# Kernel optimization log

Hardware: AMD Instinct MI355X
Metric: run time of the kernel (lower is better)

The kernel has to match this reference:

```python
import jax, jax.numpy as jnp
import numpy as np

FRACTION = 0.33  # from attn_type='query_selector_0.33'


def setup_inputs() -> dict:
    key = jax.random.key(0)
    k1, k2, k3, k4 = jax.random.split(key, 4)
    B, L, DIM_VAL, DIM_ATTN = 8, 4096, 64, 64
    scale = 1.0 / np.sqrt(DIM_VAL).astype(np.float32)
    x = jax.random.normal(k1, (B, L, DIM_VAL), dtype=jnp.float32)
    Wq = jax.random.normal(k2, (DIM_VAL, DIM_ATTN), dtype=jnp.float32) * scale
    Wk = jax.random.normal(k3, (DIM_VAL, DIM_ATTN), dtype=jnp.float32) * scale
    Wv = jax.random.normal(k4, (DIM_VAL, DIM_VAL), dtype=jnp.float32) * scale
    return {"x": x, "Wq": Wq, "Wk": Wk, "Wv": Wv}


def reference(x, Wq, Wk, Wv):
    # Projections (bias-free Linears)
    Q = jnp.einsum('bld,de->ble', x, Wq)  # [B, L, Da]
    K = jnp.einsum('bld,de->ble', x, Wk)  # [B, L, Da]
    V = jnp.einsum('bld,de->ble', x, Wv)  # [B, L, Dv]

    B, L_Q, Da = Q.shape
    l_Q = int((1.0 - FRACTION) * L_Q)  # static: shapes known at trace time

    # keys.topk(l_Q, dim=1).values -> per-channel top-l_Q along seq; mean over them
    K_top = jax.lax.top_k(jnp.swapaxes(K, 1, 2), l_Q)[0]  # [B, Da, l_Q]
    K_reduce = K_top.mean(axis=-1)                         # [B, Da]

    # score each query against the reduced key; pick top-l_Q queries
    sqk = jnp.einsum('bd,bld->bl', K_reduce, Q)            # [B, L_Q]
    indices = jax.lax.top_k(sqk, l_Q)[1]                   # [B, l_Q] int32

    # gather sampled queries
    Q_sample = jnp.take_along_axis(Q, indices[:, :, None], axis=1)  # [B, l_Q, Da]

    # dense attention for the sampled queries only
    scores = jnp.einsum('bqd,bkd->bqk', Q_sample, K) / jnp.sqrt(jnp.asarray(Da, Q.dtype))
    attn = jax.nn.softmax(scores, axis=-1)                 # [B, l_Q, L]
    out_sel = jnp.einsum('bqk,bkv->bqv', attn, V)          # [B, l_Q, Dv]

    # mean-filled result, scatter attention outputs to selected rows
    mean_values = V.mean(axis=-2)                          # [B, Dv]
    result = jnp.broadcast_to(mean_values[:, None, :], (B, L_Q, V.shape[-1]))
    result = result.at[jnp.arange(B)[:, None], indices].set(out_sel)
    return result
```

## Files before the change

### kernel.cpp

```cpp
#include <hip/hip_runtime.h>
#include <hip/hip_bf16.h>
#include <math.h>

#define BATCH 8
#define SEQ   4096
#define DIM   64
#define LQ    2744
#define QPB   128
#define NQB   22
#define QPAD  2816
#define KS    4
#define QSC   0.1803368801111204f

typedef _Float16 half8 __attribute__((ext_vector_type(8)));
typedef short    bs8   __attribute__((ext_vector_type(8)));
typedef float    fx16  __attribute__((ext_vector_type(16)));
typedef unsigned short ushort_t;

union UH { uint4 u4; half8 h; };
union UB { unsigned u[4]; uint4 u4; bs8 s; };

__device__ __forceinline__ unsigned pack_bf16(float a, float b) {
    __hip_bfloat162 h = __float22bfloat162_rn(make_float2(a, b));
    union { __hip_bfloat162 h; unsigned u; } cv; cv.h = h; return cv.u;
}

__device__ __forceinline__ unsigned f2sort(float f) {
    unsigned u = __float_as_uint(f);
    return (u & 0x80000000u) ? ~u : (u | 0x80000000u);
}
__device__ __forceinline__ float sort2f(unsigned u) {
    return __uint_as_float((u & 0x80000000u) ? (u & 0x7FFFFFFFu) : ~u);
}

struct RadSh {
    unsigned u[4096];
    unsigned hist[256];
    unsigned wsum[4];
    unsigned res[2];
    float    rsum[4];
    int      eq[256];
    int      cnts[2];
};

__device__ void radix_select_4096(const unsigned* u, int k, unsigned* hist,
                                  unsigned* wsum, unsigned* res, int pass_lo) {
    const int t = threadIdx.x;
    const int lane = t & 63, wv = t >> 6;
    if (t == 0) { res[0] = 0u; res[1] = (unsigned)k; }
    for (int pass = 3; pass >= pass_lo; --pass) {
        const int shift = pass * 8;
        hist[t] = 0u;
        __syncthreads();
        const unsigned pref  = res[0];
        const unsigned kk    = res[1];
        const unsigned hmask = (pass == 3) ? 0u : (0xFFFFFFFFu << (shift + 8));
        for (int i = t; i < 4096; i += 256) {
            unsigned ui = u[i];
            if ((ui & hmask) == pref) atomicAdd(&hist[(ui >> shift) & 255u], 1u);
        }
        __syncthreads();
        const unsigned h = hist[t];
        unsigned s = h;
#pragma unroll
        for (int ofs = 1; ofs < 64; ofs <<= 1) {
            unsigned a = __shfl_down(s, ofs, 64);
            s += (lane + ofs < 64) ? a : 0u;
        }
        if (lane == 0) wsum[wv] = s;
        __syncthreads();
#pragma unroll
        for (int w2 = 0; w2 < 4; ++w2)
            if (w2 > wv) s += wsum[w2];
        if (s >= kk && (s - h) < kk) {
            res[0] = pref | ((unsigned)t << shift);
            res[1] = kk - (s - h);
        }
        __syncthreads();
    }
}

__global__ __launch_bounds__(256) void proj_kernel(
    const float* __restrict__ x,  const float* __restrict__ Wq,
    const float* __restrict__ Wk, const float* __restrict__ Wv,
    float* __restrict__ Q, float* __restrict__ Kt,
    _Float16* __restrict__ Qh, _Float16* __restrict__ Kh,
    ushort_t* __restrict__ Vt, float* __restrict__ pmean) {
    const int rt = blockIdx.x, b = blockIdx.y, t = threadIdx.x;
    __shared__ float  red[4][64];
    const int ch = t & 63, rg = t >> 6;
    const float* xb = x + (size_t)b * SEQ * DIM;
    float accq[16], acck[16], accv[16];
#pragma unroll
    for (int i = 0; i < 16; ++i) { accq[i] = 0.f; acck[i] = 0.f; accv[i] = 0.f; }
    for (int dc = 0; dc < 4; ++dc) {
        float wq[16], wk[16], wv[16];
#pragma unroll
        for (int dd = 0; dd < 16; ++dd) {
            int d = dc * 16 + dd;
            wq[dd] = Wq[d * 64 + ch]; wk[dd] = Wk[d * 64 + ch]; wv[dd] = Wv[d * 64 + ch];
        }
        for (int r = 0; r < 16; ++r) {
            const int off = (rt * 64 + rg * 16 + r) * DIM + dc * 16;
            const float* xrow =
                xb + (unsigned)__builtin_amdgcn_readfirstlane(off);
            float xv[16];
#pragma unroll
            for (int dd = 0; dd < 16; ++dd) xv[dd] = xrow[dd];
#pragma unroll
            for (int dd = 0; dd < 16; ++dd) {
                accq[r] = fmaf(xv[dd], wq[dd], accq[r]);
                acck[r] = fmaf(xv[dd], wk[dd], acck[r]);
                accv[r] = fmaf(xv[dd], wv[dd], accv[r]);
            }
        }
    }
    const int rowbase = rt * 64 + rg * 16;
    float sv = 0.f;
#pragma unroll
    for (int r = 0; r < 16; ++r) {
        size_t o = ((size_t)b * SEQ + rowbase + r) * DIM + ch;
        Q[o]  = accq[r];
        Qh[o] = (_Float16)(accq[r] * QSC);
        Kh[o] = (_Float16)acck[r];
        sv += accv[r];
    }
    float4* ktp = (float4*)(Kt + ((size_t)b * 64 + ch) * SEQ + rowbase);
    ktp[0] = make_float4(acck[0], acck[1], acck[2], acck[3]);
    ktp[1] = make_float4(acck[4], acck[5], acck[6], acck[7]);
    ktp[2] = make_float4(acck[8], acck[9], acck[10], acck[11]);
    ktp[3] = make_float4(acck[12], acck[13], acck[14], acck[15]);
    {
        unsigned pk[8];
#pragma unroll
        for (int i = 0; i < 8; ++i) pk[i] = pack_bf16(accv[2*i], accv[2*i+1]);
        uint4* vp = (uint4*)(Vt + ((size_t)(b * 64 + ch)) * SEQ + rowbase);
        vp[0] = make_uint4(pk[0], pk[1], pk[4], pk[5]);
        vp[1] = make_uint4(pk[2], pk[3], pk[6], pk[7]);
    }
    red[rg][ch] = sv;
    __syncthreads();
    if (rg == 0)
        pmean[((size_t)b * 64 + ch) * 64 + rt] =
            red[0][ch] + red[1][ch] + red[2][ch] + red[3][ch];
}

__global__ __launch_bounds__(256) void kmean_kernel(const float* __restrict__ Kt,
                                                    const float* __restrict__ pmean,
                                                    float* __restrict__ Kred,
                                                    float* __restrict__ meanfin) {
    __shared__ RadSh sh;
    const int bc = blockIdx.x, t = threadIdx.x;
    if (t < 64) {
        float v = pmean[(size_t)bc * 64 + t];
        for (int m = 1; m < 64; m <<= 1) v += __shfl_xor(v, m, 64);
        if (t == 0) meanfin[bc] = v * (1.0f / (float)SEQ);
    }
    const float4* c4 = (const float4*)(Kt + (size_t)bc * SEQ);
    for (int i = t; i < 1024; i += 256) {
        float4 v = c4[i];
        sh.u[i*4+0] = f2sort(v.x); sh.u[i*4+1] = f2sort(v.y);
        sh.u[i*4+2] = f2sort(v.z); sh.u[i*4+3] = f2sort(v.w);
    }
    __syncthreads();
    radix_select_4096(sh.u, LQ, sh.hist, sh.wsum, sh.res, 2);
    const unsigned Tu = sh.res[0];
    const int krem = (int)sh.res[1];
    float loc = 0.f;
    for (int i = t; i < 4096; i += 256)
        if ((sh.u[i] & 0xFFFF0000u) > Tu) loc += sort2f(sh.u[i]);
    for (int msk = 1; msk < 64; msk <<= 1) loc += __shfl_xor(loc, msk, 64);
    if ((t & 63) == 0) sh.rsum[t >> 6] = loc;
    __syncthreads();
    if (t == 0) {
        float s = sh.rsum[0] + sh.rsum[1] + sh.rsum[2] + sh.rsum[3]
                + (float)krem * sort2f(Tu | 0x8000u);
        Kred[bc] = s / (float)LQ;
    }
}

__global__ __launch_bounds__(256) void sqk_kernel(const float* __restrict__ Q,
                                                  const float* __restrict__ Kred,
                                                  float* __restrict__ sqk,
                                                  float4* __restrict__ pz) {
    const int b = blockIdx.y, l = blockIdx.x * 256 + threadIdx.x;
    __shared__ float kr[64];
    if (threadIdx.x < 64) kr[threadIdx.x] = Kred[b * 64 + threadIdx.x];
    {
        const int tid = (blockIdx.y * 16 + blockIdx.x) * 256 + threadIdx.x;
        const float4 z = make_float4(0.f, 0.f, 0.f, 0.f);
        for (int i = tid; i < 366080; i += 32768) pz[i] = z;
    }
    __syncthreads();
    const float4* q = (const float4*)(Q + ((size_t)b * SEQ + l) * DIM);
    float s = 0.f;
#pragma unroll
    for (int i = 0; i < 16; ++i) {
        float4 v = q[i];
        s = fmaf(v.x, kr[i*4+0], s); s = fmaf(v.y, kr[i*4+1], s);
        s = fmaf(v.z, kr[i*4+2], s); s = fmaf(v.w, kr[i*4+3], s);
    }
    sqk[b * SEQ + l] = s;
}

__global__ __launch_bounds__(256) void select_kernel(const float* __restrict__ sqk,
                                                     int* __restrict__ sel,
                                                     int* __restrict__ inv) {
    __shared__ RadSh r;
    const int b = blockIdx.x, t = threadIdx.x;
    const float* col = sqk + (size_t)b * SEQ;
    int* invb = inv + (size_t)b * SEQ;
    for (int i = t; i < 4096; i += 256) {
        r.u[i] = f2sort(col[i]);
        invb[i] = -1;
    }
    if (t < 2) r.cnts[t] = 0;
    __syncthreads();
    radix_select_4096(r.u, LQ, r.hist, r.wsum, r.res, 0);
    const unsigned Tu = r.res[0];
    const int krem = (int)r.res[1];
    int* selb = sel + b * QPAD;
    for (int i = t; i < 4096; i += 256) {
        unsigned ui = r.u[i];
        if (ui > Tu) {
            int p = atomicAdd(&r.cnts[0], 1);
            selb[p] = i;
            invb[i] = p;
        } else if (ui == Tu) {
            int p = atomicAdd(&r.cnts[1], 1);
            if (p < 256) r.eq[p] = i;
        }
    }
    __syncthreads();
    if (t == 0) {
        int ng = r.cnts[0];
        int ne = r.cnts[1] < 256 ? r.cnts[1] : 256;
        for (int i = 1; i < ne; ++i) {
            int v = r.eq[i], j = i - 1;
            while (j >= 0 && r.eq[j] > v) { r.eq[j+1] = r.eq[j]; --j; }
            r.eq[j+1] = v;
        }
        for (int j = 0; j < krem; ++j) {
            selb[ng + j] = r.eq[j];
            invb[r.eq[j]] = ng + j;
        }
    }
    __syncthreads();
    if (t < QPAD - LQ) selb[LQ + t] = selb[LQ - 1];
}

__global__ __launch_bounds__(256, 3) void attn_kernel(
    const ushort_t* __restrict__ Qh, const ushort_t* __restrict__ Kh,
    const ushort_t* __restrict__ Vt, const int* __restrict__ sel,
    float* __restrict__ pl, float* __restrict__ pout) {
    const int qt = blockIdx.x, ks = blockIdx.y, b = blockIdx.z;
    const int t = threadIdx.x, w = t >> 6, lane = t & 63;
    const int col = lane & 31, h = lane >> 5;

    __shared__ ushort_t Ktile[2][32 * 64];
    __shared__ ushort_t Vtile[2][32 * 64];

    half8 qf[4];
    {
        const int q = qt * QPB + w * 32 + col;
        const int row = sel[b * QPAD + q];
        const uint4* qg = (const uint4*)(Qh + ((size_t)b * SEQ + row) * DIM);
#pragma unroll
        for (int m = 0; m < 4; ++m) { UH u; u.u4 = qg[2 * m + h]; qf[m] = u.h; }
    }

    int koff[4], voff[4];
#pragma unroll
    for (int m = 0; m < 4; ++m)
        koff[m] = col * 64 + 8 * ((2 * m + h) ^ (col & 7));
#pragma unroll
    for (int i = 0; i < 4; ++i)
        voff[i] = col * 64 + 8 * ((i * 2 + h) ^ (col & 7));

    fx16 O0, O1;
#pragma unroll
    for (int r = 0; r < 16; ++r) { O0[r] = 0.f; O1[r] = 0.f; }
    float l = 0.f;

    const int srow = t >> 3, sgr = t & 7;
    const int lg = sgr ^ (srow & 7);
    const int vD = lg >> 2, vc = (lg >> 1) & 1, vh = lg & 1;
    const size_t kgbase = ((size_t)b * SEQ + ks * 1024 + srow) * DIM + 8 * lg;
    const size_t vgbase = ((size_t)(b * DIM + srow + 32 * vD)) * SEQ
                          + ks * 1024 + vc * 16 + vh * 8;

    const int sw = srow * 64 + sgr * 8;

    auto step = [&](int buf) {
        fx16 S;
#pragma unroll
        for (int r = 0; r < 16; ++r) S[r] = 0.f;
#pragma unroll
        for (int m = 0; m < 4; ++m) {
            UH kf;
            kf.u4 = *(const uint4*)&Ktile[buf][koff[m]];
            S = __builtin_amdgcn_mfma_f32_32x32x16_f16(kf.h, qf[m], S, 0, 0, 0);
        }
        float p[16];
#pragma unroll
        for (int r = 0; r < 16; ++r) p[r] = exp2f(S[r]);
#pragma unroll
        for (int r = 0; r < 16; ++r) l += p[r];
        UB A0, A1;
#pragma unroll
        for (int v = 0; v < 4; ++v) {
            A0.u[v] = pack_bf16(p[2 * v],     p[2 * v + 1]);
            A1.u[v] = pack_bf16(p[8 + 2 * v], p[8 + 2 * v + 1]);
        }
#pragma unroll
        for (int D = 0; D < 2; ++D) {
            fx16& O = D ? O1 : O0;
#pragma unroll
            for (int c = 0; c < 2; ++c) {
                UB vf;
                vf.u4 = *(const uint4*)&Vtile[buf][voff[D * 2 + c]];
                O = __builtin_amdgcn_mfma_f32_32x32x16_bf16(c ? A1.s : A0.s, vf.s,
                                                            O, 0, 0, 0);
            }
        }
    };

    uint4 kA = *(const uint4*)(Kh + kgbase);
    uint4 vA = *(const uint4*)(Vt + vgbase);
    uint4 kB = *(const uint4*)(Kh + kgbase + 32 * DIM);
    uint4 vB = *(const uint4*)(Vt + vgbase + 32);

    for (int tile = 0; tile < 32; tile += 2) {
        *(uint4*)&Ktile[0][sw] = kA;
        *(uint4*)&Vtile[0][sw] = vA;
        __syncthreads();
        if (tile + 2 < 32) {
            kA = *(const uint4*)(Kh + kgbase + (size_t)(tile + 2) * 32 * DIM);
            vA = *(const uint4*)(Vt + vgbase + (size_t)(tile + 2) * 32);
        }
        step(0);
        *(uint4*)&Ktile[1][sw] = kB;
        *(uint4*)&Vtile[1][sw] = vB;
        __syncthreads();
        if (tile + 3 < 32) {
            kB = *(const uint4*)(Kh + kgbase + (size_t)(tile + 3) * 32 * DIM);
            vB = *(const uint4*)(Vt + vgbase + (size_t)(tile + 3) * 32);
        }
        step(1);
    }

    l += __shfl_xor(l, 32);

    const int qg0 = qt * QPB + w * 32;
    const size_t base = (size_t)b * QPAD + qg0;
#pragma unroll
    for (int D = 0; D < 2; ++D) {
        const fx16& O = D ? O1 : O0;
#pragma unroll
        for (int r = 0; r < 16; ++r) {
            const int q = (r & 3) + 8 * (r >> 2) + 4 * h;
            atomicAdd(&pout[(base + q) * DIM + D * 32 + col], O[r]);
        }
    }
    if (h == 0) atomicAdd(&pl[base + col], l);
}

__global__ __launch_bounds__(256) void comb_kernel(
    const float* __restrict__ pl, const float* __restrict__ pout,
    const int* __restrict__ inv, const float* __restrict__ meanfin,
    float* __restrict__ out) {
    const int idx = blockIdx.x * 256 + threadIdx.x;
    const int b = idx >> 16;
    const int rc = idx & 65535;
    const int row = rc >> 4, c = rc & 15;
    const int p = inv[b * SEQ + row];
    float4 o;
    if (p >= 0) {
        const size_t s0 = (size_t)b * QPAD + p;
        const float invl = 1.0f / pl[s0];
        float4 a = ((const float4*)(pout + s0 * DIM))[c];
        o = make_float4(a.x * invl, a.y * invl, a.z * invl, a.w * invl);
    } else {
        o = make_float4(meanfin[b * 64 + c * 4 + 0], meanfin[b * 64 + c * 4 + 1],
                        meanfin[b * 64 + c * 4 + 2], meanfin[b * 64 + c * 4 + 3]);
    }
    ((float4*)out)[idx] = o;
}

extern "C" void kernel_launch(void* const* d_in, const int* in_sizes, int n_in,
                              void* d_out, int out_size, void* d_ws, size_t ws_size,
                              hipStream_t stream) {
    const float* x  = (const float*)d_in[0];
    const float* Wq = (const float*)d_in[1];
    const float* Wk = (const float*)d_in[2];
    const float* Wv = (const float*)d_in[3];
    float* out = (float*)d_out;
    char* wsb  = (char*)d_ws;

    float*    Q       = (float*)(wsb);
    _Float16* Qh      = (_Float16*)(wsb + 8388608);
    _Float16* Kh      = (_Float16*)(wsb + 12582912);
    ushort_t* Vt      = (ushort_t*)(wsb + 16777216);
    float*    pmean   = (float*)(wsb + 20971520);
    float*    meanfin = (float*)(wsb + 21102592);
    float*    Kred    = (float*)(wsb + 21104640);
    float*    sqk     = (float*)(wsb + 21106688);
    int*      sel     = (int*)(wsb + 21237760);
    int*      inv     = (int*)(wsb + 21327872);
    float*    Kt      = (float*)(wsb + 21458944);
    float*    pout    = (float*)(wsb + 21458944);
    float*    pl      = (float*)(wsb + 21458944 + 5767168);

    proj_kernel  <<<dim3(64, 8),          256, 0, stream>>>(x, Wq, Wk, Wv, Q, Kt,
                                                            Qh, Kh, Vt, pmean);
    kmean_kernel <<<512,                  256, 0, stream>>>(Kt, pmean, Kred, meanfin);
    sqk_kernel   <<<dim3(16, 8),          256, 0, stream>>>(Q, Kred, sqk,
                                                            (float4*)pout);
    select_kernel<<<8,                    256, 0, stream>>>(sqk, sel, inv);
    attn_kernel  <<<dim3(NQB, KS, BATCH), 256, 0, stream>>>((const ushort_t*)Qh,
                                                            (const ushort_t*)Kh,
                                                            Vt, sel, pl, pout);
    comb_kernel  <<<2048,                 256, 0, stream>>>(pl, pout, inv, meanfin, out);
}
```

Baseline: 183.3 us.

## Fuse query scoring into selection kernel and move zero-fill into kmean

The separate sqk and select kernels become one 1024-thread-per-batch kernel. It computes the query scores directly into shared memory and runs the radix select there, so the global sqk buffer and one launch go away. The radix select now takes a configurable thread count. Zeroing of the partial-output buffer moves into kmean_kernel: each block clears the Kt slice it has already copied to shared memory, which aliases pout. The attention step also starts its first MFMA from a zero register instead of a cleared accumulator and sums the row probabilities as a tree. The cost is that the score computation now runs on only 8 blocks, which may limit the memory bandwidth available for reading Q.

```diff
diff --git a/kernel.cpp b/kernel.cpp
--- a/kernel.cpp
+++ b/kernel.cpp
@@ -44,37 +44,43 @@
 };
 
 __device__ void radix_select_4096(const unsigned* u, int k, unsigned* hist,
-                                  unsigned* wsum, unsigned* res, int pass_lo) {
+                                  unsigned* wsum, unsigned* res, int pass_lo,
+                                  int NT) {
     const int t = threadIdx.x;
     const int lane = t & 63, wv = t >> 6;
     if (t == 0) { res[0] = 0u; res[1] = (unsigned)k; }
     for (int pass = 3; pass >= pass_lo; --pass) {
         const int shift = pass * 8;
-        hist[t] = 0u;
+        if (t < 256) hist[t] = 0u;
         __syncthreads();
         const unsigned pref  = res[0];
         const unsigned kk    = res[1];
         const unsigned hmask = (pass == 3) ? 0u : (0xFFFFFFFFu << (shift + 8));
-        for (int i = t; i < 4096; i += 256) {
+        for (int i = t; i < 4096; i += NT) {
             unsigned ui = u[i];
             if ((ui & hmask) == pref) atomicAdd(&hist[(ui >> shift) & 255u], 1u);
         }
         __syncthreads();
-        const unsigned h = hist[t];
-        unsigned s = h;
-#pragma unroll
-        for (int ofs = 1; ofs < 64; ofs <<= 1) {
-            unsigned a = __shfl_down(s, ofs, 64);
-            s += (lane + ofs < 64) ? a : 0u;
-        }
-        if (lane == 0) wsum[wv] = s;
-        __syncthreads();
-#pragma unroll
-        for (int w2 = 0; w2 < 4; ++w2)
-            if (w2 > wv) s += wsum[w2];
-        if (s >= kk && (s - h) < kk) {
-            res[0] = pref | ((unsigned)t << shift);
-            res[1] = kk - (s - h);
+        unsigned h = 0u, s = 0u;
+        if (t < 256) {
+            h = hist[t];
+            s = h;
+#pragma unroll
+            for (int ofs = 1; ofs < 64; ofs <<= 1) {
+                unsigned a = __shfl_down(s, ofs, 64);
+                s += (lane + ofs < 64) ? a : 0u;
+            }
+            if (lane == 0) wsum[wv] = s;
+        }
+        __syncthreads();
+        if (t < 256) {
+#pragma unroll
+            for (int w2 = 0; w2 < 4; ++w2)
+                if (w2 > wv) s += wsum[w2];
+            if (s >= kk && (s - h) < kk) {
+                res[0] = pref | ((unsigned)t << shift);
+                res[1] = kk - (s - h);
+            }
         }
         __syncthreads();
     }
@@ -145,7 +151,7 @@
             red[0][ch] + red[1][ch] + red[2][ch] + red[3][ch];
 }
 
-__global__ __launch_bounds__(256) void kmean_kernel(const float* __restrict__ Kt,
+__global__ __launch_bounds__(256) void kmean_kernel(float* __restrict__ Kt,
                                                     const float* __restrict__ pmean,
                                                     float* __restrict__ Kred,
                                                     float* __restrict__ meanfin) {
@@ -163,7 +169,12 @@
         sh.u[i*4+2] = f2sort(v.z); sh.u[i*4+3] = f2sort(v.w);
     }
     __syncthreads();
-    radix_select_4096(sh.u, LQ, sh.hist, sh.wsum, sh.res, 2);
+    {
+        float4* pz = (float4*)Kt + (size_t)bc * 1024;
+        const float4 z = make_float4(0.f, 0.f, 0.f, 0.f);
+        for (int i = t; i < 1024; i += 256) pz[i] = z;
+    }
+    radix_select_4096(sh.u, LQ, sh.hist, sh.wsum, sh.res, 2, 256);
     const unsigned Tu = sh.res[0];
     const int krem = (int)sh.res[1];
     float loc = 0.f;
@@ -179,48 +190,35 @@
     }
 }
 
-__global__ __launch_bounds__(256) void sqk_kernel(const float* __restrict__ Q,
-                                                  const float* __restrict__ Kred,
-                                                  float* __restrict__ sqk,
-                                                  float4* __restrict__ pz) {
-    const int b = blockIdx.y, l = blockIdx.x * 256 + threadIdx.x;
+__global__ __launch_bounds__(1024) void sqk_select_kernel(
+    const float* __restrict__ Q, const float* __restrict__ Kred,
+    int* __restrict__ sel, int* __restrict__ inv) {
+    __shared__ RadSh r;
     __shared__ float kr[64];
-    if (threadIdx.x < 64) kr[threadIdx.x] = Kred[b * 64 + threadIdx.x];
-    {
-        const int tid = (blockIdx.y * 16 + blockIdx.x) * 256 + threadIdx.x;
-        const float4 z = make_float4(0.f, 0.f, 0.f, 0.f);
-        for (int i = tid; i < 366080; i += 32768) pz[i] = z;
-    }
-    __syncthreads();
-    const float4* q = (const float4*)(Q + ((size_t)b * SEQ + l) * DIM);
-    float s = 0.f;
-#pragma unroll
-    for (int i = 0; i < 16; ++i) {
-        float4 v = q[i];
-        s = fmaf(v.x, kr[i*4+0], s); s = fmaf(v.y, kr[i*4+1], s);
-        s = fmaf(v.z, kr[i*4+2], s); s = fmaf(v.w, kr[i*4+3], s);
-    }
-    sqk[b * SEQ + l] = s;
-}
-
-__global__ __launch_bounds__(256) void select_kernel(const float* __restrict__ sqk,
-                                                     int* __restrict__ sel,
-                                                     int* __restrict__ inv) {
-    __shared__ RadSh r;
     const int b = blockIdx.x, t = threadIdx.x;
-    const float* col = sqk + (size_t)b * SEQ;
+    if (t < 64) kr[t] = Kred[b * 64 + t];
     int* invb = inv + (size_t)b * SEQ;
-    for (int i = t; i < 4096; i += 256) {
-        r.u[i] = f2sort(col[i]);
-        invb[i] = -1;
+    __syncthreads();
+    for (int j = 0; j < 4; ++j) {
+        const int l = t + 1024 * j;
+        const float4* q = (const float4*)(Q + ((size_t)b * SEQ + l) * DIM);
+        float s = 0.f;
+#pragma unroll
+        for (int i = 0; i < 16; ++i) {
+            float4 v = q[i];
+            s = fmaf(v.x, kr[i*4+0], s); s = fmaf(v.y, kr[i*4+1], s);
+            s = fmaf(v.z, kr[i*4+2], s); s = fmaf(v.w, kr[i*4+3], s);
+        }
+        r.u[l] = f2sort(s);
+        invb[l] = -1;
     }
     if (t < 2) r.cnts[t] = 0;
     __syncthreads();
-    radix_select_4096(r.u, LQ, r.hist, r.wsum, r.res, 0);
+    radix_select_4096(r.u, LQ, r.hist, r.wsum, r.res, 0, 1024);
     const unsigned Tu = r.res[0];
     const int krem = (int)r.res[1];
     int* selb = sel + b * QPAD;
-    for (int i = t; i < 4096; i += 256) {
+    for (int i = t; i < 4096; i += 1024) {
         unsigned ui = r.u[i];
         if (ui > Tu) {
             int p = atomicAdd(&r.cnts[0], 1);
@@ -277,9 +275,9 @@
     for (int i = 0; i < 4; ++i)
         voff[i] = col * 64 + 8 * ((i * 2 + h) ^ (col & 7));
 
-    fx16 O0, O1;
-#pragma unroll
-    for (int r = 0; r < 16; ++r) { O0[r] = 0.f; O1[r] = 0.f; }
+    fx16 O0, O1, Zf;
+#pragma unroll
+    for (int r = 0; r < 16; ++r) { O0[r] = 0.f; O1[r] = 0.f; Zf[r] = 0.f; }
     float l = 0.f;
 
     const int srow = t >> 3, sgr = t & 7;
@@ -292,11 +290,10 @@
     const int sw = srow * 64 + sgr * 8;
 
     auto step = [&](int buf) {
-        fx16 S;
-#pragma unroll
-        for (int r = 0; r < 16; ++r) S[r] = 0.f;
-#pragma unroll
-        for (int m = 0; m < 4; ++m) {
+        UH kf0; kf0.u4 = *(const uint4*)&Ktile[buf][koff[0]];
+        fx16 S = __builtin_amdgcn_mfma_f32_32x32x16_f16(kf0.h, qf[0], Zf, 0, 0, 0);
+#pragma unroll
+        for (int m = 1; m < 4; ++m) {
             UH kf;
             kf.u4 = *(const uint4*)&Ktile[buf][koff[m]];
             S = __builtin_amdgcn_mfma_f32_32x32x16_f16(kf.h, qf[m], S, 0, 0, 0);
@@ -304,8 +301,13 @@
         float p[16];
 #pragma unroll
         for (int r = 0; r < 16; ++r) p[r] = exp2f(S[r]);
-#pragma unroll
-        for (int r = 0; r < 16; ++r) l += p[r];
+        {
+            float l01 = (p[0] + p[1]) + (p[2] + p[3]);
+            float l23 = (p[4] + p[5]) + (p[6] + p[7]);
+            float l45 = (p[8] + p[9]) + (p[10] + p[11]);
+            float l67 = (p[12] + p[13]) + (p[14] + p[15]);
+            l += (l01 + l23) + (l45 + l67);
+        }
         UB A0, A1;
 #pragma unroll
         for (int v = 0; v < 4; ++v) {
@@ -404,7 +406,6 @@
     float*    pmean   = (float*)(wsb + 20971520);
     float*    meanfin = (float*)(wsb + 21102592);
     float*    Kred    = (float*)(wsb + 21104640);
-    float*    sqk     = (float*)(wsb + 21106688);
     int*      sel     = (int*)(wsb + 21237760);
     int*      inv     = (int*)(wsb + 21327872);
     float*    Kt      = (float*)(wsb + 21458944);
@@ -414,9 +415,7 @@
     proj_kernel  <<<dim3(64, 8),          256, 0, stream>>>(x, Wq, Wk, Wv, Q, Kt,
                                                             Qh, Kh, Vt, pmean);
     kmean_kernel <<<512,                  256, 0, stream>>>(Kt, pmean, Kred, meanfin);
-    sqk_kernel   <<<dim3(16, 8),          256, 0, stream>>>(Q, Kred, sqk,
-                                                            (float4*)pout);
-    select_kernel<<<8,                    256, 0, stream>>>(sqk, sel, inv);
+    sqk_select_kernel<<<8,               1024, 0, stream>>>(Q, Kred, sel, inv);
     attn_kernel  <<<dim3(NQB, KS, BATCH), 256, 0, stream>>>((const ushort_t*)Qh,
                                                             (const ushort_t*)Kh,
                                                             Vt, sel, pl, pout);
```

Measured after the change: 215.0 us. 17.3% more time.

## Fuse combine step into attention via last-block scatter and mean prefill

Applied to the files above, without the earlier changes.

Removes the separate combine kernel and the inverse-index array. The sqk kernel now prefills the output with per-batch column means. The last attention block to finish each query tile, tracked by an atomic counter stored in the reused sqk buffer, normalizes the tile and scatters it into the selected rows. Zeroing of the partial-sum buffers moves from sqk_kernel into kmean_kernel, which overwrites its own Kt column after loading it. Minor tweaks add a tree-shaped row-sum and seed the first MFMA with a zero accumulator. In exchange the attention tail gains a threadfence, an extra barrier and a serialized epilogue.

```diff
diff --git a/kernel.cpp b/kernel.cpp
--- a/kernel.cpp
+++ b/kernel.cpp
@@ -145,7 +145,7 @@
             red[0][ch] + red[1][ch] + red[2][ch] + red[3][ch];
 }
 
-__global__ __launch_bounds__(256) void kmean_kernel(const float* __restrict__ Kt,
+__global__ __launch_bounds__(256) void kmean_kernel(float* __restrict__ Kt,
                                                     const float* __restrict__ pmean,
                                                     float* __restrict__ Kred,
                                                     float* __restrict__ meanfin) {
@@ -163,6 +163,11 @@
         sh.u[i*4+2] = f2sort(v.z); sh.u[i*4+3] = f2sort(v.w);
     }
     __syncthreads();
+    {
+        float4* pz = (float4*)Kt + (size_t)bc * 1024;
+        const float4 z = make_float4(0.f, 0.f, 0.f, 0.f);
+        for (int i = t; i < 1024; i += 256) pz[i] = z;
+    }
     radix_select_4096(sh.u, LQ, sh.hist, sh.wsum, sh.res, 2);
     const unsigned Tu = sh.res[0];
     const int krem = (int)sh.res[1];
@@ -182,15 +187,14 @@
 __global__ __launch_bounds__(256) void sqk_kernel(const float* __restrict__ Q,
                                                   const float* __restrict__ Kred,
                                                   float* __restrict__ sqk,
-                                                  float4* __restrict__ pz) {
+                                                  const float* __restrict__ meanf,
+                                                  float* __restrict__ out) {
     const int b = blockIdx.y, l = blockIdx.x * 256 + threadIdx.x;
     __shared__ float kr[64];
+    __shared__ float4 mf4[16];
     if (threadIdx.x < 64) kr[threadIdx.x] = Kred[b * 64 + threadIdx.x];
-    {
-        const int tid = (blockIdx.y * 16 + blockIdx.x) * 256 + threadIdx.x;
-        const float4 z = make_float4(0.f, 0.f, 0.f, 0.f);
-        for (int i = tid; i < 366080; i += 32768) pz[i] = z;
-    }
+    if (threadIdx.x < 16)
+        mf4[threadIdx.x] = ((const float4*)(meanf + b * 64))[threadIdx.x];
     __syncthreads();
     const float4* q = (const float4*)(Q + ((size_t)b * SEQ + l) * DIM);
     float s = 0.f;
@@ -201,21 +205,20 @@
         s = fmaf(v.z, kr[i*4+2], s); s = fmaf(v.w, kr[i*4+3], s);
     }
     sqk[b * SEQ + l] = s;
-}
-
-__global__ __launch_bounds__(256) void select_kernel(const float* __restrict__ sqk,
-                                                     int* __restrict__ sel,
-                                                     int* __restrict__ inv) {
+    float4* orow = (float4*)(out + ((size_t)b * SEQ + l) * DIM);
+#pragma unroll
+    for (int c = 0; c < 16; ++c) orow[c] = mf4[c];
+}
+
+__global__ __launch_bounds__(256) void select_kernel(float* __restrict__ sqk,
+                                                     int* __restrict__ sel) {
     __shared__ RadSh r;
     const int b = blockIdx.x, t = threadIdx.x;
     const float* col = sqk + (size_t)b * SEQ;
-    int* invb = inv + (size_t)b * SEQ;
-    for (int i = t; i < 4096; i += 256) {
-        r.u[i] = f2sort(col[i]);
-        invb[i] = -1;
-    }
+    for (int i = t; i < 4096; i += 256) r.u[i] = f2sort(col[i]);
     if (t < 2) r.cnts[t] = 0;
     __syncthreads();
+    if (t < NQB) ((int*)(sqk + (size_t)b * SEQ))[t] = 0;
     radix_select_4096(r.u, LQ, r.hist, r.wsum, r.res, 0);
     const unsigned Tu = r.res[0];
     const int krem = (int)r.res[1];
@@ -225,7 +228,6 @@
         if (ui > Tu) {
             int p = atomicAdd(&r.cnts[0], 1);
             selb[p] = i;
-            invb[i] = p;
         } else if (ui == Tu) {
             int p = atomicAdd(&r.cnts[1], 1);
             if (p < 256) r.eq[p] = i;
@@ -240,10 +242,7 @@
             while (j >= 0 && r.eq[j] > v) { r.eq[j+1] = r.eq[j]; --j; }
             r.eq[j+1] = v;
         }
-        for (int j = 0; j < krem; ++j) {
-            selb[ng + j] = r.eq[j];
-            invb[r.eq[j]] = ng + j;
-        }
+        for (int j = 0; j < krem; ++j) selb[ng + j] = r.eq[j];
     }
     __syncthreads();
     if (t < QPAD - LQ) selb[LQ + t] = selb[LQ - 1];
@@ -252,13 +251,15 @@
 __global__ __launch_bounds__(256, 3) void attn_kernel(
     const ushort_t* __restrict__ Qh, const ushort_t* __restrict__ Kh,
     const ushort_t* __restrict__ Vt, const int* __restrict__ sel,
-    float* __restrict__ pl, float* __restrict__ pout) {
+    float* __restrict__ pl, float* __restrict__ pout,
+    int* __restrict__ cnt, float* __restrict__ out) {
     const int qt = blockIdx.x, ks = blockIdx.y, b = blockIdx.z;
     const int t = threadIdx.x, w = t >> 6, lane = t & 63;
     const int col = lane & 31, h = lane >> 5;
 
     __shared__ ushort_t Ktile[2][32 * 64];
     __shared__ ushort_t Vtile[2][32 * 64];
+    __shared__ int amlast;
 
     half8 qf[4];
     {
@@ -277,9 +278,9 @@
     for (int i = 0; i < 4; ++i)
         voff[i] = col * 64 + 8 * ((i * 2 + h) ^ (col & 7));
 
-    fx16 O0, O1;
-#pragma unroll
-    for (int r = 0; r < 16; ++r) { O0[r] = 0.f; O1[r] = 0.f; }
+    fx16 O0, O1, Zf;
+#pragma unroll
+    for (int r = 0; r < 16; ++r) { O0[r] = 0.f; O1[r] = 0.f; Zf[r] = 0.f; }
     float l = 0.f;
 
     const int srow = t >> 3, sgr = t & 7;
@@ -292,11 +293,10 @@
     const int sw = srow * 64 + sgr * 8;
 
     auto step = [&](int buf) {
-        fx16 S;
-#pragma unroll
-        for (int r = 0; r < 16; ++r) S[r] = 0.f;
-#pragma unroll
-        for (int m = 0; m < 4; ++m) {
+        UH kf0; kf0.u4 = *(const uint4*)&Ktile[buf][koff[0]];
+        fx16 S = __builtin_amdgcn_mfma_f32_32x32x16_f16(kf0.h, qf[0], Zf, 0, 0, 0);
+#pragma unroll
+        for (int m = 1; m < 4; ++m) {
             UH kf;
             kf.u4 = *(const uint4*)&Ktile[buf][koff[m]];
             S = __builtin_amdgcn_mfma_f32_32x32x16_f16(kf.h, qf[m], S, 0, 0, 0);
@@ -304,8 +304,13 @@
         float p[16];
 #pragma unroll
         for (int r = 0; r < 16; ++r) p[r] = exp2f(S[r]);
-#pragma unroll
-        for (int r = 0; r < 16; ++r) l += p[r];
+        {
+            float l01 = (p[0] + p[1]) + (p[2] + p[3]);
+            float l23 = (p[4] + p[5]) + (p[6] + p[7]);
+            float l45 = (p[8] + p[9]) + (p[10] + p[11]);
+            float l67 = (p[12] + p[13]) + (p[14] + p[15]);
+            l += (l01 + l23) + (l45 + l67);
+        }
         UB A0, A1;
 #pragma unroll
         for (int v = 0; v < 4; ++v) {
@@ -363,28 +368,23 @@
         }
     }
     if (h == 0) atomicAdd(&pl[base + col], l);
-}
-
-__global__ __launch_bounds__(256) void comb_kernel(
-    const float* __restrict__ pl, const float* __restrict__ pout,
-    const int* __restrict__ inv, const float* __restrict__ meanfin,
-    float* __restrict__ out) {
-    const int idx = blockIdx.x * 256 + threadIdx.x;
-    const int b = idx >> 16;
-    const int rc = idx & 65535;
-    const int row = rc >> 4, c = rc & 15;
-    const int p = inv[b * SEQ + row];
-    float4 o;
-    if (p >= 0) {
-        const size_t s0 = (size_t)b * QPAD + p;
+
+    __threadfence();
+    __syncthreads();
+    if (t == 0) amlast = (atomicAdd(&cnt[b * SEQ + qt], 1) == KS - 1);
+    __syncthreads();
+    if (!amlast) return;
+
+    const size_t qb0 = (size_t)b * QPAD + qt * QPB;
+    for (int idx = t; idx < QPB * 16; idx += 256) {
+        const int q = idx >> 4, c = idx & 15;
+        const size_t s0 = qb0 + q;
         const float invl = 1.0f / pl[s0];
         float4 a = ((const float4*)(pout + s0 * DIM))[c];
-        o = make_float4(a.x * invl, a.y * invl, a.z * invl, a.w * invl);
-    } else {
-        o = make_float4(meanfin[b * 64 + c * 4 + 0], meanfin[b * 64 + c * 4 + 1],
-                        meanfin[b * 64 + c * 4 + 2], meanfin[b * 64 + c * 4 + 3]);
-    }
-    ((float4*)out)[idx] = o;
+        const int row = sel[b * QPAD + qt * QPB + q];
+        ((float4*)(out + ((size_t)b * SEQ + row) * DIM))[c] =
+            make_float4(a.x * invl, a.y * invl, a.z * invl, a.w * invl);
+    }
 }
 
 extern "C" void kernel_launch(void* const* d_in, const int* in_sizes, int n_in,
@@ -406,7 +406,6 @@
     float*    Kred    = (float*)(wsb + 21104640);
     float*    sqk     = (float*)(wsb + 21106688);
     int*      sel     = (int*)(wsb + 21237760);
-    int*      inv     = (int*)(wsb + 21327872);
     float*    Kt      = (float*)(wsb + 21458944);
     float*    pout    = (float*)(wsb + 21458944);
     float*    pl      = (float*)(wsb + 21458944 + 5767168);
@@ -415,10 +414,10 @@
                                                             Qh, Kh, Vt, pmean);
     kmean_kernel <<<512,                  256, 0, stream>>>(Kt, pmean, Kred, meanfin);
     sqk_kernel   <<<dim3(16, 8),          256, 0, stream>>>(Q, Kred, sqk,
-                                                            (float4*)pout);
-    select_kernel<<<8,                    256, 0, stream>>>(sqk, sel, inv);
+                                                            meanfin, out);
+    select_kernel<<<8,                    256, 0, stream>>>(sqk, sel);
     attn_kernel  <<<dim3(NQB, KS, BATCH), 256, 0, stream>>>((const ushort_t*)Qh,
                                                             (const ushort_t*)Kh,
-                                                            Vt, sel, pl, pout);
-    comb_kernel  <<<2048,                 256, 0, stream>>>(pl, pout, inv, meanfin, out);
-}
+                                                            Vt, sel, pl, pout,
+                                                            (int*)sqk, out);
+}
```

Result: slower. 229.8 us (+25.4%).

## Run attention as single-wave blocks of 32 queries without barriers

Applied to the files above, without the earlier changes.

Each attention block is now one 64-lane wave handling 32 selected queries instead of four waves sharing 128 queries. The wave loads its own K/V tiles into double-buffered LDS with a register prefetch of the next tile, so all __syncthreads barriers go away. Query padding and the workspace sizes are shrunk to match the new 32-query granularity. In exchange, K/V tiles are no longer shared across four waves, so each wave issues four times the global/L2 loads for the same keys.

```diff
diff --git a/kernel.cpp b/kernel.cpp
--- a/kernel.cpp
+++ b/kernel.cpp
@@ -6,9 +6,9 @@
 #define SEQ   4096
 #define DIM   64
 #define LQ    2744
-#define QPB   128
-#define NQB   22
-#define QPAD  2816
+#define QPB   32
+#define NQB   86
+#define QPAD  2752
 #define KS    4
 #define QSC   0.1803368801111204f
 
@@ -189,7 +189,7 @@
     {
         const int tid = (blockIdx.y * 16 + blockIdx.x) * 256 + threadIdx.x;
         const float4 z = make_float4(0.f, 0.f, 0.f, 0.f);
-        for (int i = tid; i < 366080; i += 32768) pz[i] = z;
+        for (int i = tid; i < 357760; i += 32768) pz[i] = z;
     }
     __syncthreads();
     const float4* q = (const float4*)(Q + ((size_t)b * SEQ + l) * DIM);
@@ -249,12 +249,12 @@
     if (t < QPAD - LQ) selb[LQ + t] = selb[LQ - 1];
 }
 
-__global__ __launch_bounds__(256, 3) void attn_kernel(
+__global__ __launch_bounds__(64) void attn_kernel(
     const ushort_t* __restrict__ Qh, const ushort_t* __restrict__ Kh,
     const ushort_t* __restrict__ Vt, const int* __restrict__ sel,
     float* __restrict__ pl, float* __restrict__ pout) {
     const int qt = blockIdx.x, ks = blockIdx.y, b = blockIdx.z;
-    const int t = threadIdx.x, w = t >> 6, lane = t & 63;
+    const int lane = threadIdx.x;
     const int col = lane & 31, h = lane >> 5;
 
     __shared__ ushort_t Ktile[2][32 * 64];
@@ -262,7 +262,7 @@
 
     half8 qf[4];
     {
-        const int q = qt * QPB + w * 32 + col;
+        const int q = qt * QPB + col;
         const int row = sel[b * QPAD + q];
         const uint4* qg = (const uint4*)(Qh + ((size_t)b * SEQ + row) * DIM);
 #pragma unroll
@@ -282,13 +282,12 @@
     for (int r = 0; r < 16; ++r) { O0[r] = 0.f; O1[r] = 0.f; }
     float l = 0.f;
 
-    const int srow = t >> 3, sgr = t & 7;
-    const int lg = sgr ^ (srow & 7);
+    const int srow = lane >> 3, sgr = lane & 7;
+    const int lg = sgr ^ srow;
     const int vD = lg >> 2, vc = (lg >> 1) & 1, vh = lg & 1;
     const size_t kgbase = ((size_t)b * SEQ + ks * 1024 + srow) * DIM + 8 * lg;
     const size_t vgbase = ((size_t)(b * DIM + srow + 32 * vD)) * SEQ
                           + ks * 1024 + vc * 16 + vh * 8;
-
     const int sw = srow * 64 + sgr * 8;
 
     auto step = [&](int buf) {
@@ -325,34 +324,43 @@
         }
     };
 
-    uint4 kA = *(const uint4*)(Kh + kgbase);
-    uint4 vA = *(const uint4*)(Vt + vgbase);
-    uint4 kB = *(const uint4*)(Kh + kgbase + 32 * DIM);
-    uint4 vB = *(const uint4*)(Vt + vgbase + 32);
-
-    for (int tile = 0; tile < 32; tile += 2) {
-        *(uint4*)&Ktile[0][sw] = kA;
-        *(uint4*)&Vtile[0][sw] = vA;
-        __syncthreads();
-        if (tile + 2 < 32) {
-            kA = *(const uint4*)(Kh + kgbase + (size_t)(tile + 2) * 32 * DIM);
-            vA = *(const uint4*)(Vt + vgbase + (size_t)(tile + 2) * 32);
-        }
-        step(0);
-        *(uint4*)&Ktile[1][sw] = kB;
-        *(uint4*)&Vtile[1][sw] = vB;
-        __syncthreads();
-        if (tile + 3 < 32) {
-            kB = *(const uint4*)(Kh + kgbase + (size_t)(tile + 3) * 32 * DIM);
-            vB = *(const uint4*)(Vt + vgbase + (size_t)(tile + 3) * 32);
-        }
-        step(1);
+    uint4 kR[4], vR[4];
+#pragma unroll
+    for (int i = 0; i < 4; ++i) {
+        kR[i] = *(const uint4*)(Kh + kgbase + (size_t)(8 * i) * DIM);
+        vR[i] = *(const uint4*)(Vt + vgbase + (size_t)(8 * i) * SEQ);
+    }
+#pragma unroll
+    for (int i = 0; i < 4; ++i) {
+        *(uint4*)&Ktile[0][sw + i * 512] = kR[i];
+        *(uint4*)&Vtile[0][sw + i * 512] = vR[i];
+    }
+
+    for (int tile = 0; tile < 32; ++tile) {
+        const int buf = tile & 1;
+        if (tile < 31) {
+            const size_t ko = kgbase + (size_t)(tile + 1) * 32 * DIM;
+            const size_t vo = vgbase + (size_t)(tile + 1) * 32;
+#pragma unroll
+            for (int i = 0; i < 4; ++i) {
+                kR[i] = *(const uint4*)(Kh + ko + (size_t)(8 * i) * DIM);
+                vR[i] = *(const uint4*)(Vt + vo + (size_t)(8 * i) * SEQ);
+            }
+        }
+        step(buf);
+        if (tile < 31) {
+            const int nb = buf ^ 1;
+#pragma unroll
+            for (int i = 0; i < 4; ++i) {
+                *(uint4*)&Ktile[nb][sw + i * 512] = kR[i];
+                *(uint4*)&Vtile[nb][sw + i * 512] = vR[i];
+            }
+        }
     }
 
     l += __shfl_xor(l, 32);
 
-    const int qg0 = qt * QPB + w * 32;
-    const size_t base = (size_t)b * QPAD + qg0;
+    const size_t base = (size_t)b * QPAD + qt * QPB;
 #pragma unroll
     for (int D = 0; D < 2; ++D) {
         const fx16& O = D ? O1 : O0;
@@ -409,7 +417,7 @@
     int*      inv     = (int*)(wsb + 21327872);
     float*    Kt      = (float*)(wsb + 21458944);
     float*    pout    = (float*)(wsb + 21458944);
-    float*    pl      = (float*)(wsb + 21458944 + 5767168);
+    float*    pl      = (float*)(wsb + 21458944 + 5636096);
 
     proj_kernel  <<<dim3(64, 8),          256, 0, stream>>>(x, Wq, Wk, Wv, Q, Kt,
                                                             Qh, Kh, Vt, pmean);
@@ -417,7 +425,7 @@
     sqk_kernel   <<<dim3(16, 8),          256, 0, stream>>>(Q, Kred, sqk,
                                                             (float4*)pout);
     select_kernel<<<8,                    256, 0, stream>>>(sqk, sel, inv);
-    attn_kernel  <<<dim3(NQB, KS, BATCH), 256, 0, stream>>>((const ushort_t*)Qh,
+    attn_kernel  <<<dim3(NQB, KS, BATCH),  64, 0, stream>>>((const ushort_t*)Qh,
                                                             (const ushort_t*)Kh,
                                                             Vt, sel, pl, pout);
     comb_kernel  <<<2048,                 256, 0, stream>>>(pl, pout, inv, meanfin, out);
```

Result: slower. 297.6 us (+62.4%).
